# Kernel optimization log

Measured on AMD Instinct MI355X. Metric: run time of the kernel, lower is better.

## Reference

```python
import jax, jax.numpy as jnp
import numpy as np

NUM_INST = 32
EPS = 1e-5


def _conv(x, w, b, stride=1, pad=0):
    y = jax.lax.conv_general_dilated(
        x, w, (stride, stride), ((pad, pad), (pad, pad)),
        dimension_numbers=('NCHW', 'OIHW', 'NCHW'))
    return y + b[None, :, None, None]


def _deconv(x, w, b):
    # torch ConvTranspose2d(k=3, s=2, p=1, output_padding=1); w is (Cin, Cout, 3, 3)
    wf = jnp.flip(w, (2, 3)).transpose(1, 0, 2, 3)  # -> OIHW
    y = jax.lax.conv_general_dilated(
        x, wf, (1, 1), ((1, 2), (1, 2)), lhs_dilation=(2, 2),
        dimension_numbers=('NCHW', 'OIHW', 'NCHW'))
    return y + b[None, :, None, None]


def _inorm(x):
    m = x.mean((2, 3), keepdims=True)
    v = x.var((2, 3), keepdims=True)  # biased, matches InstanceNorm2d
    return (x - m) * jax.lax.rsqrt(v + EPS)


def _rpad(x, p=3):
    return jnp.pad(x, ((0, 0), (0, 0), (p, p), (p, p)), mode='reflect')


def _backbone(input, w0, b0, w1, b1, w2, b2, w3, b3, w4, b4,
              w5, b5, w6, b6, w7, b7, w8, b8, w9, b9):
    x = jax.nn.relu(_inorm(_conv(_rpad(input), w0, b0)))          # [B,16,H,W]
    x = jax.nn.relu(_inorm(_conv(x, w1, b1, stride=2, pad=1)))    # [B,32,H/2,..]
    x = jax.nn.relu(_inorm(_conv(x, w2, b2, stride=2, pad=1)))    # [B,64,H/4,..]
    x = jax.nn.relu(_inorm(_conv(x, w3, b3, stride=2, pad=1)))    # [B,128,H/8,..]
    x = jax.nn.relu(_inorm(_conv(x, w4, b4, stride=2, pad=1)))    # [B,256,H/16,..]
    x = jax.nn.relu(_inorm(_deconv(x, w5, b5)))                   # [B,128,H/8,..]
    x = jax.nn.relu(_inorm(_deconv(x, w6, b6)))                   # [B,64,H/4,..]
    x = jax.nn.relu(_inorm(_deconv(x, w7, b7)))                   # [B,32,H/2,..]
    x = jax.nn.relu(_inorm(_deconv(x, w8, b8)))                   # [B,16,H,W]
    return jnp.tanh(_conv(_rpad(x), w9, b9))                      # [B,Cout,H,W]


def _segment_mean(outputs, inst):
    # outputs [B,C,H,W]; inst [B,1,H,W] int labels shared across the batch.
    B, C, H, W = outputs.shape
    seg = inst.reshape(-1)                                # [B*H*W]
    feats = outputs.transpose(0, 2, 3, 1).reshape(-1, C)  # [B*H*W, C]
    sums = jax.ops.segment_sum(feats, seg, num_segments=NUM_INST)
    counts = jax.ops.segment_sum(jnp.ones((feats.shape[0],), feats.dtype), seg,
                                 num_segments=NUM_INST)
    means = sums / jnp.maximum(counts, 1.0)[:, None]      # [NUM_INST, C]
    out = means[seg].reshape(B, H, W, C).transpose(0, 3, 1, 2)
    return out


def setup_inputs() -> dict:
    key = jax.random.key(0)
    ks = jax.random.split(key, 16)
    B, Cin, Cout, H, W = 4, 3, 3, 512, 512
    inp = {
        'input': jax.random.normal(ks[0], (B, Cin, H, W), jnp.float32),
        'inst': jax.random.randint(ks[1], (B, 1, H, W), 0, NUM_INST, jnp.int32),
    }
    std = 0.02
    # conv weights OIHW; deconv weights torch-style (Cin, Cout, kH, kW)
    shapes = [
        ('w0', (16, Cin, 7, 7)), ('w1', (32, 16, 3, 3)), ('w2', (64, 32, 3, 3)),
        ('w3', (128, 64, 3, 3)), ('w4', (256, 128, 3, 3)),
        ('w5', (256, 128, 3, 3)), ('w6', (128, 64, 3, 3)),
        ('w7', (64, 32, 3, 3)), ('w8', (32, 16, 3, 3)), ('w9', (Cout, 16, 7, 7)),
    ]
    bias_dims = [16, 32, 64, 128, 256, 128, 64, 32, 16, Cout]
    for i, (name, shp) in enumerate(shapes):
        inp[name] = std * jax.random.normal(ks[2 + i], shp, jnp.float32)
        inp['b%d' % i] = jnp.zeros((bias_dims[i],), jnp.float32)
    return inp


def reference(input, inst, w0, b0, w1, b1, w2, b2, w3, b3, w4, b4,
              w5, b5, w6, b6, w7, b7, w8, b8, w9, b9):
    outputs = _backbone(input, w0, b0, w1, b1, w2, b2, w3, b3, w4, b4,
                        w5, b5, w6, b6, w7, b7, w8, b8, w9, b9)
    return _segment_mean(outputs, inst)
```

## Files before the change

### kernel.cpp

```cpp
#include <hip/hip_runtime.h>
#include <math.h>

#define EPS_F 1e-5f

typedef __attribute__((ext_vector_type(8))) short short8;
typedef __attribute__((ext_vector_type(4))) float f32x4;
typedef __attribute__((ext_vector_type(8))) unsigned short ushort8;

__device__ __forceinline__ int reflect512(int v) {
    v = v < 0 ? -v : v;
    return v >= 512 ? 1022 - v : v;
}

__device__ __forceinline__ ushort f2bf(float f) {
    union { float f; unsigned u; } v; v.f = f;
    unsigned r = v.u + 0x7FFFu + ((v.u >> 16) & 1u);
    return (ushort)(r >> 16);
}
__device__ __forceinline__ float bf2f(ushort u) {
    union { unsigned u; float f; } v; v.u = (unsigned)u << 16;
    return v.f;
}

__device__ __forceinline__ float fast_tanh(float x) {
    float cx = fminf(fmaxf(x, -9.f), 9.f);
    float e  = __builtin_amdgcn_exp2f(cx * 2.8853900817779268f);
    return (e - 1.f) * __builtin_amdgcn_rcpf(e + 1.f);
}

template<int CIN, int COUT, bool DEC>
__device__ __forceinline__ void wp_mid(
    const float* __restrict__ w, ushort* __restrict__ dst, int i)
{
    constexpr int CIP = ((CIN + 31) / 32) * 32;
    int ci = i % CIP;
    int oc = (i / CIP) % COUT;
    int t  = i / (CIP * COUT);
    float x = 0.f;
    if (ci < CIN)
        x = DEC ? w[((size_t)ci * COUT + oc) * 9 + t]
                : w[((size_t)oc * CIN + ci) * 9 + t];
    dst[i] = f2bf(x);
}

template<bool L9>
__device__ __forceinline__ void wp_7(
    const float* __restrict__ w, ushort* __restrict__ dst, int i)
{
    int j   = i & 7;
    int oc  = (i >> 3) & 15;
    int kqe = (i >> 7) & 3;
    int cn  = i >> 9;
    float x = 0.f;
    if (L9) {
        int k = kqe * 8 + j;
        int rowsel = k >> 4, ci = k & 15;
        int p = cn / 7, tx = cn - 7 * p;
        int trow = 2 * p + rowsel;
        if (trow < 7 && oc < 3)
            x = w[((size_t)oc * 16 + ci) * 49 + trow * 7 + tx];
    } else {
        int k = cn * 32 + kqe * 8 + j;
        int t = k >> 3, ci = k & 7;
        if (t < 49 && ci < 3)
            x = w[((size_t)oc * 3 + ci) * 49 + t];
    }
    dst[i] = f2bf(x);
}

struct WprepArgs {
    const float* w[10];
    ushort* d[10];
};

__global__ __launch_bounds__(256) void wprep_all(WprepArgs a)
{
    int bi = blockIdx.x;
    int t  = threadIdx.x;
    if      (bi < 36)   wp_mid<16,  32,  false>(a.w[1], a.d[1], (bi        ) * 256 + t);
    else if (bi < 108)  wp_mid<32,  64,  false>(a.w[2], a.d[2], (bi - 36   ) * 256 + t);
    else if (bi < 396)  wp_mid<64,  128, false>(a.w[3], a.d[3], (bi - 108  ) * 256 + t);
    else if (bi < 1548) wp_mid<128, 256, false>(a.w[4], a.d[4], (bi - 396  ) * 256 + t);
    else if (bi < 2700) wp_mid<256, 128, true >(a.w[5], a.d[5], (bi - 1548 ) * 256 + t);
    else if (bi < 2988) wp_mid<128, 64,  true >(a.w[6], a.d[6], (bi - 2700 ) * 256 + t);
    else if (bi < 3060) wp_mid<64,  32,  true >(a.w[7], a.d[7], (bi - 2988 ) * 256 + t);
    else if (bi < 3078) wp_mid<32,  16,  true >(a.w[8], a.d[8], (bi - 3060 ) * 256 + t);
    else if (bi < 3104) wp_7<false>(a.w[0], a.d[0], (bi - 3078) * 256 + t);
    else                wp_7<true >(a.w[9], a.d[9], (bi - 3104) * 256 + t);
}

template<int CIN, int COUT, int WIN, int MODE, int NWN, int MSUB, int RT, int CT>
__global__ __launch_bounds__(256) void mfconv(
    const ushort* __restrict__ in, const ushort* __restrict__ wbf,
    const float* __restrict__ bias, ushort* __restrict__ out,
    const float* __restrict__ stats_in, float invHWin,
    float* __restrict__ stats_out)
{
    constexpr int HWIN = WIN * WIN;
    constexpr int WOUT = (MODE == 0) ? (WIN / 2) : (WIN * 2);
    constexpr int HWOUT = WOUT * WOUT;
    constexpr int NMG = 4 / NWN;
    constexpr int NOC = NWN * 16;
    constexpr int M = NMG * MSUB * 16;
    static_assert(M == RT * CT, "tile mismatch");
    constexpr int SPAN = (MODE == 0) ? WOUT : WIN;
    constexpr int XC = SPAN / CT, YC = SPAN / RT;
    constexpr int NG = COUT / NOC;
    constexpr int NR = (MODE == 0) ? (2 * RT + 1) : (RT + 1);
    constexpr int NCO = (MODE == 0) ? (2 * CT + 1) : (CT + 1);
    constexpr int NPIX = NR * NCO;
    constexpr int CIP = ((CIN + 31) / 32) * 32;
    constexpr int NQ = (MODE == 0) ? 1 : 4;
    constexpr int LPW = 36;
    constexpr int NPOUT = (MODE == 0 ? 1 : 4) * M;
    constexpr int NOCP = NOC + 8;

    constexpr int TDY[9] = {1,1,1,0,0,0,0,0,0};
    constexpr int TDX[9] = {1,0,0,1,0,0,1,0,0};
    constexpr int TQ [9] = {3,2,3,1,0,1,3,2,3};

    extern __shared__ ushort sa[];
    __shared__ float mrall[CIP][2];
    __shared__ float sred[4][16][2];

    const int tid = threadIdx.x;
    const int lane = tid & 63, wv = tid >> 6;
    const int ln = lane & 15, kq = lane >> 4;
    const int wn = wv % NWN, wm = wv / NWN;
    const int grp = tid & 3;

    int bi = blockIdx.x;
    const int xc = bi % XC; bi /= XC;
    const int yc = bi % YC; bi /= YC;
    const int g  = bi % NG;
    const int b  = bi / NG;

    const int ocg = g * NOC + wn * 16 + ln;
    const float b0 = bias[ocg];
    f32x4 acc[NQ][MSUB];
    #pragma unroll
    for (int q = 0; q < NQ; q++)
        #pragma unroll
        for (int s = 0; s < MSUB; s++)
            acc[q][s] = (f32x4){b0, b0, b0, b0};

    for (int e = tid; e < CIP; e += 256) {
        float m = 0.f, r = 0.f;
        if (e < CIN) {
            int c = b * CIN + e;
            float s1 = stats_in[2 * c], s2 = stats_in[2 * c + 1];
            m = s1 * invHWin;
            r = rsqrtf(fmaf(s2, invHWin, -m * m) + EPS_F);
        }
        mrall[e][0] = m; mrall[e][1] = r;
    }

    const ushort* inb = in + (size_t)b * HWIN * CIN;

    for (int c0 = 0; c0 < CIP; c0 += 32) {
        __syncthreads();
        const int ch0 = c0 + 8 * grp;
        float m8[8], r8[8];
        #pragma unroll
        for (int j = 0; j < 8; j++) { m8[j] = mrall[ch0 + j][0]; r8[j] = mrall[ch0 + j][1]; }
        for (int pix = tid >> 2; pix < NPIX; pix += 64) {
            int pr = pix / NCO, pc = pix - pr * NCO;
            int gy, gx;
            if (MODE == 0) { gy = 2 * (yc * RT) - 1 + pr; gx = 2 * (xc * CT) - 1 + pc; }
            else           { gy = yc * RT + pr;           gx = xc * CT + pc; }
            ushort8 pk;
            #pragma unroll
            for (int j = 0; j < 8; j++) pk[j] = 0;
            if ((unsigned)gy < (unsigned)WIN && (unsigned)gx < (unsigned)WIN && ch0 < CIN) {
                ushort8 raw = *(const ushort8*)(inb + (size_t)(gy * WIN + gx) * CIN + ch0);
                #pragma unroll
                for (int j = 0; j < 8; j++) {
                    float x = bf2f(raw[j]);
                    pk[j] = f2bf(fmaxf((x - m8[j]) * r8[j], 0.f));
                }
            }
            *(ushort8*)&sa[pix * LPW + grp * 8] = pk;
        }
        __syncthreads();
        #pragma unroll
        for (int t = 0; t < 9; t++) {
            short8 bfr = *(const short8*)&wbf[((size_t)t * COUT + ocg) * CIP + c0 + kq * 8];
            #pragma unroll
            for (int s = 0; s < MSUB; s++) {
                const int mb = wm * MSUB * 16 + s * 16;
                const int r = mb / CT, cb = mb % CT;
                int pix;
                if (MODE == 0) pix = (t / 3 + 2 * r) * NCO + 2 * (cb + ln) + t % 3;
                else           pix = (TDY[t] + r) * NCO + cb + ln + TDX[t];
                short8 afr = *(const short8*)&sa[pix * LPW + kq * 8];
                int qd = (MODE == 0) ? 0 : TQ[t];
                acc[qd][s] = __builtin_amdgcn_mfma_f32_16x16x32_bf16(afr, bfr, acc[qd][s], 0, 0, 0);
            }
        }
    }

    float s1 = 0.f, s2 = 0.f;
    #pragma unroll
    for (int q = 0; q < NQ; q++)
        #pragma unroll
        for (int s = 0; s < MSUB; s++)
            #pragma unroll
            for (int rg = 0; rg < 4; rg++) {
                float v = acc[q][s][rg];
                s1 += v; s2 = fmaf(v, v, s2);
            }
    s1 += __shfl_xor(s1, 16); s2 += __shfl_xor(s2, 16);
    s1 += __shfl_xor(s1, 32); s2 += __shfl_xor(s2, 32);
    if (lane < 16) { sred[wv][lane][0] = s1; sred[wv][lane][1] = s2; }

    __syncthreads();
    const int ocl = wn * 16 + ln;
    if (MODE == 0) {
        #pragma unroll
        for (int s = 0; s < MSUB; s++)
            #pragma unroll
            for (int rg = 0; rg < 4; rg++) {
                const int m = wm * MSUB * 16 + s * 16 + kq * 4 + rg;
                sa[m * NOCP + ocl] = f2bf(acc[0][s][rg]);
            }
    } else {
        #pragma unroll
        for (int q = 0; q < 4; q++) {
            const int dy = q >> 1, dx = q & 1;
            #pragma unroll
            for (int s = 0; s < MSUB; s++)
                #pragma unroll
                for (int rg = 0; rg < 4; rg++) {
                    const int m = wm * MSUB * 16 + s * 16 + kq * 4 + rg;
                    const int r = m / CT, c = m % CT;
                    const int lp = (2 * r + dy) * (2 * CT) + 2 * c + dx;
                    sa[lp * NOCP + ocl] = f2bf(acc[q][s][rg]);
                }
        }
    }
    __syncthreads();

    ushort* ob = out + (size_t)b * HWOUT * COUT + g * NOC;
    for (int e = tid; e < (NPOUT * NOC) / 8; e += 256) {
        int u = e * 8;
        int lp = u / NOC, co = u % NOC;
        int gp;
        if (MODE == 0) {
            int r = lp / CT, c = lp % CT;
            gp = (yc * RT + r) * WOUT + xc * CT + c;
        } else {
            int r2 = lp / (2 * CT), x2 = lp % (2 * CT);
            gp = (2 * (yc * RT) + r2) * WOUT + 2 * (xc * CT) + x2;
        }
        *(ushort8*)&ob[(size_t)gp * COUT + co] = *(const ushort8*)&sa[lp * NOCP + co];
    }

    if (tid < NOC) {
        int wnn = tid >> 4, oc = tid & 15;
        float t1 = 0.f, t2 = 0.f;
        #pragma unroll
        for (int k = 0; k < NMG; k++) {
            t1 += sred[wnn + k * NWN][oc][0];
            t2 += sred[wnn + k * NWN][oc][1];
        }
        int cix = b * COUT + g * NOC + wnn * 16 + oc;
        atomicAdd(&stats_out[2 * cix],     t1);
        atomicAdd(&stats_out[2 * cix + 1], t2);
    }
}

template<bool BFIN, bool SEG>
__global__ __launch_bounds__(256, 4) void conv7x(
    const float* __restrict__ inf, const ushort* __restrict__ inb16,
    const ushort* __restrict__ wpk, const float* __restrict__ bias,
    ushort* __restrict__ out,
    const float* __restrict__ stats_in, float invHWin,
    float* __restrict__ stats_out,
    const int* __restrict__ inst, float* __restrict__ segacc)
{
    constexpr int W = 512, HW = 512 * 512;
    constexpr int STR = BFIN ? 20 : 12;
    constexpr int SASZ = BFIN ? (980 * 20) : 12288;

    __shared__ ushort sa[SASZ];
    __shared__ float mr[16][2];
    __shared__ float segl[SEG ? 128 : 1];
    __shared__ float sred[4][16][2];

    const int tid = threadIdx.x;
    const int lane = tid & 63, wv = tid >> 6;
    const int ln = lane & 15, kq = lane >> 4;

    int bi = blockIdx.x;
    const int xc = bi & 7;
    const int yr = (bi >> 3) & 63;
    const int b  = bi >> 9;
    const int y0 = yr * 8, x0 = xc * 64;

    if constexpr (SEG) { if (tid < 128) segl[tid] = 0.f; }
    if constexpr (BFIN) {
        if (tid < 16) {
            int c = b * 16 + tid;
            float s1 = stats_in[2 * c], s2 = stats_in[2 * c + 1];
            float m = s1 * invHWin;
            mr[tid][0] = m;
            mr[tid][1] = rsqrtf(fmaf(s2, invHWin, -m * m) + EPS_F);
        }
        __syncthreads();
        const int h = tid & 1;
        float m8[8], r8[8];
        #pragma unroll
        for (int j = 0; j < 8; j++) { m8[j] = mr[8 * h + j][0]; r8[j] = mr[8 * h + j][1]; }
        const ushort* inb = inb16 + (size_t)b * HW * 16;
        for (int pix = tid >> 1; pix < 980; pix += 128) {
            int pr = pix / 70, pc = pix - pr * 70;
            int gy = reflect512(y0 - 3 + pr);
            int gx = reflect512(x0 - 3 + pc);
            ushort8 raw = *(const ushort8*)(inb + (size_t)(gy * W + gx) * 16 + 8 * h);
            ushort8 pk;
            #pragma unroll
            for (int j = 0; j < 8; j++) {
                float x = bf2f(raw[j]);
                pk[j] = f2bf(fmaxf((x - m8[j]) * r8[j], 0.f));
            }
            *(ushort8*)&sa[pix * STR + 8 * h] = pk;
        }
    } else {
        const float* p0 = inf + (size_t)b * 3 * HW;
        for (int pix = tid; pix < 980; pix += 256) {
            int pr = pix / 70, pc = pix - pr * 70;
            int gy = reflect512(y0 - 3 + pr);
            int gx = reflect512(x0 - 3 + pc);
            const float* p = p0 + gy * W + gx;
            ushort8 pk;
            #pragma unroll
            for (int j = 0; j < 8; j++) pk[j] = 0;
            pk[0] = f2bf(p[0]); pk[1] = f2bf(p[HW]); pk[2] = f2bf(p[2 * (size_t)HW]);
            *(ushort8*)&sa[pix * STR] = pk;
        }
    }
    __syncthreads();

    const float b0 = (ln < (BFIN ? 3 : 16)) ? bias[ln] : 0.f;
    f32x4 acc[8];
    #pragma unroll
    for (int s = 0; s < 8; s++) acc[s] = (f32x4){b0, b0, b0, b0};

    if constexpr (BFIN) {
        const int c0 = wv * 16;
        const int abase   = (((kq >> 1) * 70) + c0 + ln) * STR + (kq & 1) * 8;
        const int abase13 = (13 * 70 + c0 + ln) * STR + (kq & 1) * 8;
        const ushort* wp9 = wpk + ((size_t)kq * 16 + ln) * 8;
        #pragma unroll
        for (int tx = 0; tx < 7; tx++) {
            short8 bfr[4];
            #pragma unroll
            for (int p = 0; p < 4; p++)
                bfr[p] = *(const short8*)(wp9 + (size_t)(p * 7 + tx) * 512);
            #pragma unroll
            for (int R = 0; R < 14; R++) {
                short8 afr = (R < 13)
                    ? *(const short8*)&sa[abase + (R * 70 + tx) * STR]
                    : *(const short8*)&sa[abase13 + tx * STR];
                #pragma unroll
                for (int p = 0; p < 4; p++) {
                    const int s = R - 2 * p;
                    if (s >= 0 && s < 8)
                        acc[s] = __builtin_amdgcn_mfma_f32_16x16x32_bf16(afr, bfr[p], acc[s], 0, 0, 0);
                }
            }
        }
    } else {
        for (int cn = 0; cn < 13; cn++) {
            short8 bfr = *(const short8*)&wpk[((size_t)(cn * 4 + kq) * 16 + ln) * 8];
            int t = 4 * cn + kq;
            t = t > 48 ? 48 : t;
            const int ty = t / 7, tx = t - ty * 7;
            #pragma unroll
            for (int s = 0; s < 8; s++) {
                int m = wv * 128 + s * 16 + ln;
                int r = m >> 6, c = m & 63;
                short8 afr = *(const short8*)&sa[((r + ty) * 70 + c + tx) * STR];
                acc[s] = __builtin_amdgcn_mfma_f32_16x16x32_bf16(afr, bfr, acc[s], 0, 0, 0);
            }
        }
    }

    if constexpr (SEG) {
        float* sf = (float*)sa;
        __syncthreads();
        if (ln < 3) {
            #pragma unroll
            for (int s = 0; s < 8; s++)
                #pragma unroll
                for (int rg = 0; rg < 4; rg++) {
                    int m = s * 64 + wv * 16 + kq * 4 + rg;
                    sf[m * 5 + ln] = acc[s][rg];
                }
        }
        __syncthreads();
        const int* ib = inst + ((size_t)b << 18);
        for (int p2 = tid; p2 < 512; p2 += 256) {
            int r = p2 >> 6, c = p2 & 63;
            int lab = ib[(y0 + r) * W + x0 + c] & 31;
            atomicAdd(&segl[lab * 4 + 0], fast_tanh(sf[p2 * 5 + 0]));
            atomicAdd(&segl[lab * 4 + 1], fast_tanh(sf[p2 * 5 + 1]));
            atomicAdd(&segl[lab * 4 + 2], fast_tanh(sf[p2 * 5 + 2]));
            atomicAdd(&segl[lab * 4 + 3], 1.f);
        }
        __syncthreads();
        if (tid < 128) {
            float v = segl[tid];
            if (v != 0.f) atomicAdd(&segacc[tid], v);
        }
    } else {
        float s1 = 0.f, s2 = 0.f;
        #pragma unroll
        for (int s = 0; s < 8; s++)
            #pragma unroll
            for (int rg = 0; rg < 4; rg++) {
                float v = acc[s][rg];
                s1 += v; s2 = fmaf(v, v, s2);
            }
        s1 += __shfl_xor(s1, 16); s2 += __shfl_xor(s2, 16);
        s1 += __shfl_xor(s1, 32); s2 += __shfl_xor(s2, 32);
        if (lane < 16) { sred[wv][lane][0] = s1; sred[wv][lane][1] = s2; }

        __syncthreads();
        #pragma unroll
        for (int s = 0; s < 8; s++)
            #pragma unroll
            for (int rg = 0; rg < 4; rg++) {
                int m = wv * 128 + s * 16 + kq * 4 + rg;
                sa[m * 24 + ln] = f2bf(acc[s][rg]);
            }
        __syncthreads();
        ushort* ob = out + (size_t)b * HW * 16;
        for (int e = tid; e < 1024; e += 256) {
            int u = e * 8;
            int lp = u >> 4, co = u & 15;
            int gp = (y0 + (lp >> 6)) * W + x0 + (lp & 63);
            *(ushort8*)&ob[(size_t)gp * 16 + co] = *(const ushort8*)&sa[lp * 24 + co];
        }
        if (tid < 16) {
            float t1 = 0.f, t2 = 0.f;
            #pragma unroll
            for (int k = 0; k < 4; k++) { t1 += sred[k][tid][0]; t2 += sred[k][tid][1]; }
            int cix = b * 16 + tid;
            atomicAdd(&stats_out[2 * cix],     t1);
            atomicAdd(&stats_out[2 * cix + 1], t2);
        }
    }
}

#define HW9 262144
__global__ void seg_final(const float* __restrict__ acc, float* __restrict__ means)
{
    int i = threadIdx.x;
    if (i < 96) {
        int s = i / 3, c = i - s * 3;
        means[i] = acc[s * 4 + c] / fmaxf(acc[s * 4 + 3], 1.f);
    }
}

__global__ __launch_bounds__(256) void seg_scatter(
    const int* __restrict__ inst, const float* __restrict__ means,
    float* __restrict__ out)
{
    int p   = blockIdx.x * 256 + threadIdx.x;
    int b   = p >> 18;
    int r   = p & (HW9 - 1);
    int lab = inst[p] & 31;
    float* ob = out + (size_t)b * 3 * HW9;
    ob[r]           = means[lab * 3 + 0];
    ob[HW9 + r]     = means[lab * 3 + 1];
    ob[2 * HW9 + r] = means[lab * 3 + 2];
}

extern "C" void kernel_launch(void* const* d_in, const int* in_sizes, int n_in,
                              void* d_out, int out_size, void* d_ws, size_t ws_size,
                              hipStream_t stream)
{
    const float* x_in = (const float*)d_in[0];
    const int*   inst = (const int*)d_in[1];
    const float* W_[10];
    const float* Bs[10];
    for (int i = 0; i < 10; i++) {
        W_[i] = (const float*)d_in[2 + 2 * i];
        Bs[i] = (const float*)d_in[3 + 2 * i];
    }
    float* out = (float*)d_out;

    ushort* Ab  = (ushort*)d_ws;
    ushort* Bb2 = Ab + (size_t)16777216;
    float*  st  = (float*)(Bb2 + (size_t)8388608);
    const int coff[9] = {0, 128, 384, 896, 1920, 3968, 4992, 5504, 5760};
    float* s_[9];
    for (int i = 0; i < 9; i++) s_[i] = st + coff[i];
    float* segacc = st + 5888;
    float* means  = st + 6016;
    ushort* wb = (ushort*)(st + 8192);
    const size_t OW1 = 0, OW2 = 9216, OW3 = 27648, OW4 = 101376,
                 OW5 = 396288, OW6 = 691200, OW7 = 764928, OW8 = 783360;
    ushort* wb0 = wb + 790000;
    ushort* wb9 = wb0 + 6656;

    hipMemsetAsync(st, 0, 6016 * sizeof(float), stream);

    WprepArgs wa;
    for (int i = 0; i < 10; i++) wa.w[i] = W_[i];
    wa.d[0] = wb0;
    wa.d[1] = wb + OW1; wa.d[2] = wb + OW2; wa.d[3] = wb + OW3; wa.d[4] = wb + OW4;
    wa.d[5] = wb + OW5; wa.d[6] = wb + OW6; wa.d[7] = wb + OW7; wa.d[8] = wb + OW8;
    wa.d[9] = wb9;
    wprep_all<<<dim3(3160), dim3(256), 0, stream>>>(wa);

    conv7x<false, false><<<dim3(2048), dim3(256), 0, stream>>>(
        x_in, nullptr, wb0, Bs[0], Ab, nullptr, 0.f, s_[0], nullptr, nullptr);

    mfconv<16, 32, 512, 0, 2, 4, 4, 32><<<dim3(2048), dim3(256), 42120, stream>>>(
        Ab, wb + OW1, Bs[1], Bb2, s_[0], 1.f / 262144.f, s_[1]);

    mfconv<32, 64, 256, 0, 2, 4, 4, 32><<<dim3(1024), dim3(256), 42120, stream>>>(
        Bb2, wb + OW2, Bs[2], Ab, s_[1], 1.f / 65536.f, s_[2]);

    mfconv<64, 128, 128, 0, 2, 4, 4, 32><<<dim3(512), dim3(256), 42120, stream>>>(
        Ab, wb + OW3, Bs[3], Bb2, s_[2], 1.f / 16384.f, s_[3]);

    mfconv<128, 256, 64, 0, 2, 2, 2, 32><<<dim3(512), dim3(256), 23400, stream>>>(
        Bb2, wb + OW4, Bs[4], Ab, s_[3], 1.f / 4096.f, s_[4]);

    mfconv<256, 128, 32, 1, 1, 1, 2, 32><<<dim3(512), dim3(256), 12288, stream>>>(
        Ab, wb + OW5, Bs[5], Bb2, s_[4], 1.f / 1024.f, s_[5]);

    mfconv<128, 64, 64, 1, 2, 2, 2, 32><<<dim3(512), dim3(256), 20480, stream>>>(
        Bb2, wb + OW6, Bs[6], Ab, s_[5], 1.f / 4096.f, s_[6]);

    mfconv<64, 32, 128, 1, 2, 2, 2, 32><<<dim3(1024), dim3(256), 20480, stream>>>(
        Ab, wb + OW7, Bs[7], Bb2, s_[6], 1.f / 16384.f, s_[7]);

    mfconv<32, 16, 256, 1, 1, 2, 2, 64><<<dim3(2048), dim3(256), 24576, stream>>>(
        Bb2, wb + OW8, Bs[8], Ab, s_[7], 1.f / 65536.f, s_[8]);

    conv7x<true, true><<<dim3(2048), dim3(256), 0, stream>>>(
        nullptr, Ab, wb9, Bs[9], nullptr, s_[8], 1.f / 262144.f, nullptr, inst, segacc);

    seg_final<<<dim3(1), dim3(96), 0, stream>>>(segacc, means);
    seg_scatter<<<dim3(4096), dim3(256), 0, stream>>>(inst, means, out);
}
```

Measured before the change: 504.7 us.

## Add specialized layer-1 conv packing two taps per K=32 MFMA

Adds a dedicated kernel for the 16-to-32 channel stride-2 conv. Its weights are repacked so each K=32 MFMA step covers two 3x3 taps of 16 channels each, instead of padding 16 channels to 32. This halves the wasted MFMA work and shrinks shared memory from 42120 to 23400 bytes, which may allow more resident blocks. The input tile is loaded with fused instance-norm and ReLU. The weight prep kernel is re-indexed to match the smaller packed buffer, which risks layout mistakes.

```diff
diff --git a/kernel.cpp b/kernel.cpp
--- a/kernel.cpp
+++ b/kernel.cpp
@@ -40,6 +40,18 @@
     if (ci < CIN)
         x = DEC ? w[((size_t)ci * COUT + oc) * 9 + t]
                 : w[((size_t)oc * CIN + ci) * 9 + t];
+    dst[i] = f2bf(x);
+}
+
+__device__ __forceinline__ void wp_l1(
+    const float* __restrict__ w, ushort* __restrict__ dst, int i)
+{
+    int k  = i & 31;
+    int oc = (i >> 5) & 31;
+    int c  = i >> 10;
+    int tapsel = k >> 4, ci = k & 15;
+    int t = 2 * c + tapsel;
+    float x = (t < 9) ? w[((size_t)oc * 16 + ci) * 9 + t] : 0.f;
     dst[i] = f2bf(x);
 }
 
@@ -77,16 +89,16 @@
 {
     int bi = blockIdx.x;
     int t  = threadIdx.x;
-    if      (bi < 36)   wp_mid<16,  32,  false>(a.w[1], a.d[1], (bi        ) * 256 + t);
-    else if (bi < 108)  wp_mid<32,  64,  false>(a.w[2], a.d[2], (bi - 36   ) * 256 + t);
-    else if (bi < 396)  wp_mid<64,  128, false>(a.w[3], a.d[3], (bi - 108  ) * 256 + t);
-    else if (bi < 1548) wp_mid<128, 256, false>(a.w[4], a.d[4], (bi - 396  ) * 256 + t);
-    else if (bi < 2700) wp_mid<256, 128, true >(a.w[5], a.d[5], (bi - 1548 ) * 256 + t);
-    else if (bi < 2988) wp_mid<128, 64,  true >(a.w[6], a.d[6], (bi - 2700 ) * 256 + t);
-    else if (bi < 3060) wp_mid<64,  32,  true >(a.w[7], a.d[7], (bi - 2988 ) * 256 + t);
-    else if (bi < 3078) wp_mid<32,  16,  true >(a.w[8], a.d[8], (bi - 3060 ) * 256 + t);
-    else if (bi < 3104) wp_7<false>(a.w[0], a.d[0], (bi - 3078) * 256 + t);
-    else                wp_7<true >(a.w[9], a.d[9], (bi - 3104) * 256 + t);
+    if      (bi < 20)   wp_l1(a.w[1], a.d[1], (bi        ) * 256 + t);
+    else if (bi < 92)   wp_mid<32,  64,  false>(a.w[2], a.d[2], (bi - 20   ) * 256 + t);
+    else if (bi < 380)  wp_mid<64,  128, false>(a.w[3], a.d[3], (bi - 92   ) * 256 + t);
+    else if (bi < 1532) wp_mid<128, 256, false>(a.w[4], a.d[4], (bi - 380  ) * 256 + t);
+    else if (bi < 2684) wp_mid<256, 128, true >(a.w[5], a.d[5], (bi - 1532 ) * 256 + t);
+    else if (bi < 2972) wp_mid<128, 64,  true >(a.w[6], a.d[6], (bi - 2684 ) * 256 + t);
+    else if (bi < 3044) wp_mid<64,  32,  true >(a.w[7], a.d[7], (bi - 2972 ) * 256 + t);
+    else if (bi < 3062) wp_mid<32,  16,  true >(a.w[8], a.d[8], (bi - 3044 ) * 256 + t);
+    else if (bi < 3088) wp_7<false>(a.w[0], a.d[0], (bi - 3062) * 256 + t);
+    else                wp_7<true >(a.w[9], a.d[9], (bi - 3088) * 256 + t);
 }
 
 template<int CIN, int COUT, int WIN, int MODE, int NWN, int MSUB, int RT, int CT>
@@ -269,6 +281,149 @@
     }
 }
 
+__global__ __launch_bounds__(256) void mfconv_l1(
+    const ushort* __restrict__ in, const ushort* __restrict__ wbf,
+    const float* __restrict__ bias, ushort* __restrict__ out,
+    const float* __restrict__ stats_in, float invHWin,
+    float* __restrict__ stats_out)
+{
+    constexpr int WIN = 512, HWIN = WIN * WIN;
+    constexpr int WOUT = 256, HWOUT = WOUT * WOUT;
+    constexpr int COUT = 32, RT = 4, CT = 32;
+    constexpr int NCO = 65, NPIX = 585;
+    constexpr int LPW = 20;
+    constexpr int NOCP = 40;
+
+    extern __shared__ ushort sa[];
+    __shared__ float mrall[16][2];
+    __shared__ float sred[4][16][2];
+
+    const int tid = threadIdx.x;
+    const int lane = tid & 63, wv = tid >> 6;
+    const int ln = lane & 15, kq = lane >> 4;
+    const int wn = wv & 1, wm = wv >> 1;
+
+    int bi = blockIdx.x;
+    const int xc = bi & 7;
+    const int yc = (bi >> 3) & 63;
+    const int b  = bi >> 9;
+
+    const int ocg = wn * 16 + ln;
+    const float b0 = bias[ocg];
+    f32x4 acc[4];
+    #pragma unroll
+    for (int s = 0; s < 4; s++) acc[s] = (f32x4){b0, b0, b0, b0};
+
+    if (tid < 16) {
+        int c = b * 16 + tid;
+        float s1 = stats_in[2 * c], s2 = stats_in[2 * c + 1];
+        float m = s1 * invHWin;
+        mrall[tid][0] = m;
+        mrall[tid][1] = rsqrtf(fmaf(s2, invHWin, -m * m) + EPS_F);
+    }
+
+    const int grp = tid & 1, p0 = tid >> 1;
+    const ushort* inb = in + (size_t)b * HWIN * 16 + grp * 8;
+    ushort8 rw[5];
+    bool ok[5];
+    #pragma unroll
+    for (int i = 0; i < 5; i++) {
+        int pix = p0 + i * 128;
+        int pr = pix / NCO, pc = pix - pr * NCO;
+        int gy = 2 * (yc * RT) - 1 + pr;
+        int gx = 2 * (xc * CT) - 1 + pc;
+        ok[i] = (pix < NPIX) && ((unsigned)gy < (unsigned)WIN)
+                             && ((unsigned)gx < (unsigned)WIN);
+        if (ok[i])
+            rw[i] = *(const ushort8*)(inb + (size_t)(gy * WIN + gx) * 16);
+    }
+    __syncthreads();
+
+    float m8[8], r8[8];
+    #pragma unroll
+    for (int j = 0; j < 8; j++) {
+        m8[j] = mrall[grp * 8 + j][0];
+        r8[j] = mrall[grp * 8 + j][1];
+    }
+    #pragma unroll
+    for (int i = 0; i < 5; i++) {
+        int pix = p0 + i * 128;
+        if (pix < NPIX) {
+            ushort8 pk;
+            #pragma unroll
+            for (int j = 0; j < 8; j++) pk[j] = 0;
+            if (ok[i]) {
+                #pragma unroll
+                for (int j = 0; j < 8; j++) {
+                    float x = bf2f(rw[i][j]);
+                    pk[j] = f2bf(fmaxf((x - m8[j]) * r8[j], 0.f));
+                }
+            }
+            *(ushort8*)&sa[pix * LPW + grp * 8] = pk;
+        }
+    }
+    __syncthreads();
+
+    const int tp = kq >> 1, off8 = (kq & 1) * 8;
+    #pragma unroll
+    for (int c = 0; c < 5; c++) {
+        short8 bfr = *(const short8*)&wbf[(size_t)(c * COUT + ocg) * 32 + kq * 8];
+        int t = 2 * c + tp; t = t > 8 ? 8 : t;
+        const int ty = t / 3, tx = t - 3 * ty;
+        #pragma unroll
+        for (int s = 0; s < 4; s++) {
+            const int mb = wm * 64 + s * 16;
+            const int r = mb >> 5, cb = mb & 31;
+            short8 afr = *(const short8*)
+                &sa[((ty + 2 * r) * NCO + 2 * (cb + ln) + tx) * LPW + off8];
+            acc[s] = __builtin_amdgcn_mfma_f32_16x16x32_bf16(afr, bfr, acc[s], 0, 0, 0);
+        }
+    }
+
+    float s1 = 0.f, s2 = 0.f;
+    #pragma unroll
+    for (int s = 0; s < 4; s++)
+        #pragma unroll
+        for (int rg = 0; rg < 4; rg++) {
+            float v = acc[s][rg];
+            s1 += v; s2 = fmaf(v, v, s2);
+        }
+    s1 += __shfl_xor(s1, 16); s2 += __shfl_xor(s2, 16);
+    s1 += __shfl_xor(s1, 32); s2 += __shfl_xor(s2, 32);
+    if (lane < 16) { sred[wv][lane][0] = s1; sred[wv][lane][1] = s2; }
+
+    __syncthreads();
+    const int ocl = wn * 16 + ln;
+    #pragma unroll
+    for (int s = 0; s < 4; s++)
+        #pragma unroll
+        for (int rg = 0; rg < 4; rg++) {
+            const int m = wm * 64 + s * 16 + kq * 4 + rg;
+            sa[m * NOCP + ocl] = f2bf(acc[s][rg]);
+        }
+    __syncthreads();
+    ushort* ob = out + (size_t)b * HWOUT * COUT;
+    for (int e = tid; e < 512; e += 256) {
+        int u = e * 8;
+        int lp = u >> 5, co = u & 31;
+        int r = lp >> 5, c = lp & 31;
+        int gp = (yc * RT + r) * WOUT + xc * CT + c;
+        *(ushort8*)&ob[(size_t)gp * COUT + co] = *(const ushort8*)&sa[lp * NOCP + co];
+    }
+    if (tid < 32) {
+        int wnn = tid >> 4, oc = tid & 15;
+        float t1 = 0.f, t2 = 0.f;
+        #pragma unroll
+        for (int k = 0; k < 2; k++) {
+            t1 += sred[wnn + k * 2][oc][0];
+            t2 += sred[wnn + k * 2][oc][1];
+        }
+        int cix = b * COUT + wnn * 16 + oc;
+        atomicAdd(&stats_out[2 * cix],     t1);
+        atomicAdd(&stats_out[2 * cix + 1], t2);
+    }
+}
+
 template<bool BFIN, bool SEG>
 __global__ __launch_bounds__(256, 4) void conv7x(
     const float* __restrict__ inf, const ushort* __restrict__ inb16,
@@ -513,12 +668,12 @@
     wa.d[1] = wb + OW1; wa.d[2] = wb + OW2; wa.d[3] = wb + OW3; wa.d[4] = wb + OW4;
     wa.d[5] = wb + OW5; wa.d[6] = wb + OW6; wa.d[7] = wb + OW7; wa.d[8] = wb + OW8;
     wa.d[9] = wb9;
-    wprep_all<<<dim3(3160), dim3(256), 0, stream>>>(wa);
+    wprep_all<<<dim3(3144), dim3(256), 0, stream>>>(wa);
 
     conv7x<false, false><<<dim3(2048), dim3(256), 0, stream>>>(
         x_in, nullptr, wb0, Bs[0], Ab, nullptr, 0.f, s_[0], nullptr, nullptr);
 
-    mfconv<16, 32, 512, 0, 2, 4, 4, 32><<<dim3(2048), dim3(256), 42120, stream>>>(
+    mfconv_l1<<<dim3(2048), dim3(256), 23400, stream>>>(
         Ab, wb + OW1, Bs[1], Bb2, s_[0], 1.f / 262144.f, s_[1]);
 
     mfconv<32, 64, 256, 0, 2, 4, 4, 32><<<dim3(1024), dim3(256), 42120, stream>>>(
```

Result: faster. 482.3 us (-4.4%).
